# Kernel tuning notes

Measured on AMD Instinct MI355X. Metric: run time of the kernel, lower is better.

The kernel has to match this reference:

```python
import math
import jax, jax.numpy as jnp
import numpy as np

B, S, D, H, M, R = 4, 2048, 512, 8, 4, 32
HD = D // H
EPS = 1e-8


def setup_inputs() -> dict:
    key = jax.random.key(0)
    ks = jax.random.split(key, 12)
    sc = 1.0 / math.sqrt(D)
    return {
        "x": jax.random.normal(ks[0], (B, S, D), jnp.float32),
        "Wq": jax.random.normal(ks[1], (D, D), jnp.float32) * sc,
        "bq": jnp.zeros((D,), jnp.float32),
        "Wk": jax.random.normal(ks[2], (D, D), jnp.float32) * sc,
        "bk": jnp.zeros((D,), jnp.float32),
        "Wv": jax.random.normal(ks[3], (D, D), jnp.float32) * sc,
        "bv": jnp.zeros((D,), jnp.float32),
        "mask1": jax.random.normal(ks[4], (M, R, S), jnp.float32) * (1.0 / math.sqrt(R)),
        "mask2": jax.random.normal(ks[5], (M, R, S), jnp.float32) * (1.0 / math.sqrt(R)),
        "Wo": jax.random.normal(ks[6], (D, D), jnp.float32) * sc,
        "bo": jnp.zeros((D,), jnp.float32),
        "roll_back": jax.random.randint(ks[7], (1, S, S), 0, S, jnp.int32),
    }


def reference(x, Wq, bq, Wk, bk, Wv, bv, mask1, mask2, Wo, bo, roll_back):
    # q, k, v: [B, H, S, HD]  (torch Linear: x @ W.T + b)
    def proj(W, b):
        return (x @ W.T + b).reshape(B, S, H, HD).transpose(0, 2, 1, 3)
    q, k, v = proj(Wq, bq), proj(Wk, bk), proj(Wv, bv)

    # learnable_mask[m,s,t] = sum_r mask1[m,r,s] * mask2[m,r,t]  -> [M, S, S]
    lm = jnp.einsum("mrs,mrt->mst", mask1, mask2)
    # gather along last dim with roll indices expanded to [M, S, S]
    idx = jnp.broadcast_to(roll_back, lm.shape)
    lm_rolled = jnp.take_along_axis(lm, idx, axis=-1)  # [M, S, S]

    # att: [B, H, S, S]
    att = jnp.einsum("bhsd,bhtd->bhst", q, k) / math.sqrt(HD)
    # group heads: [B, H/M, M, S, S] * [1, 1, M, S, S]
    att = att.reshape(B, H // M, M, S, S) * lm_rolled[None, None]
    att = att.reshape(B, H, S, S)

    # Frobenius norm over last two dims, per (batch, head)
    fro = jnp.sqrt(jnp.sum(att * att, axis=(-2, -1), keepdims=True))
    att = att / (fro + EPS)

    out = jnp.einsum("bhst,bhtd->bshd", att, v).reshape(B, S, D)
    return out @ Wo.T + bo
```

## Files before the change

kernel.cpp:

```cpp
#include <hip/hip_runtime.h>
#include <hip/hip_bf16.h>

#define NB 4
#define NS 2048
#define ND 512
#define NH 8
#define NM 4
#define NR 32
#define NHD 64

typedef short frag_ab __attribute__((ext_vector_type(8)));
typedef float frag_cd __attribute__((ext_vector_type(4)));

__device__ __forceinline__ float bf2f(short s) {
    union { unsigned u; float f; } c;
    c.u = ((unsigned)(unsigned short)s) << 16;
    return c.f;
}
__device__ __forceinline__ short f2bf(float f) {
    __hip_bfloat16 h = __float2bfloat16(f);
    union { __hip_bfloat16 h; short s; } c;
    c.h = h;
    return c.s;
}

__device__ __forceinline__ void gload16(const void* g, void* l) {
    __builtin_amdgcn_global_load_lds((const __attribute__((address_space(1))) unsigned int*)g,
                                     (__attribute__((address_space(3))) unsigned int*)l,
                                     16, 0, 0);
}

__device__ __forceinline__ void stage_tile(const short* src, size_t srcStride,
                                           char* lbase, int slot) {
    int o = slot * 16;
    int row = o >> 7;
    int cc = ((o >> 4) & 7) ^ (row & 7);
    gload16(src + (size_t)row * srcStride + cc * 8, lbase + o);
}

__device__ __forceinline__ frag_ab lds_frag(const char* lbase, int row, int cc_un) {
    int cc = cc_un ^ (row & 7);
    return *(const frag_ab*)(lbase + row * 128 + cc * 16);
}

__global__ void __launch_bounds__(256) k_cast(const float* __restrict__ in,
                                              short* __restrict__ out, int n8) {
    int i = blockIdx.x * 256 + threadIdx.x;
    if (i >= n8) return;
    const float4* p = (const float4*)in + (size_t)i * 2;
    float4 a = p[0], b = p[1];
    frag_ab o;
    o[0] = f2bf(a.x); o[1] = f2bf(a.y); o[2] = f2bf(a.z); o[3] = f2bf(a.w);
    o[4] = f2bf(b.x); o[5] = f2bf(b.y); o[6] = f2bf(b.z); o[7] = f2bf(b.w);
    ((frag_ab*)out)[i] = o;
}

__global__ void __launch_bounds__(256) k_castw(const float* __restrict__ Wq,
                                               const float* __restrict__ Wk,
                                               const float* __restrict__ Wv,
                                               const float* __restrict__ Wo,
                                               short* __restrict__ out) {
    int i = blockIdx.x * 256 + threadIdx.x;
    int which = i >> 15;
    int j = i & 32767;
    const float* src = which == 0 ? Wq : which == 1 ? Wk : which == 2 ? Wv : Wo;
    const float4* p = (const float4*)src + (size_t)j * 2;
    float4 a = p[0], b = p[1];
    frag_ab o;
    o[0] = f2bf(a.x); o[1] = f2bf(a.y); o[2] = f2bf(a.z); o[3] = f2bf(a.w);
    o[4] = f2bf(b.x); o[5] = f2bf(b.y); o[6] = f2bf(b.z); o[7] = f2bf(b.w);
    ((frag_ab*)out)[i] = o;
}

__global__ void __launch_bounds__(256) k_tcast_mask(const float* __restrict__ mask1,
                                                    const float* __restrict__ mask2,
                                                    short* __restrict__ m1t,
                                                    short* __restrict__ m2t) {
    int my = blockIdx.y;
    const float* in = my < 4 ? mask1 : mask2;
    short* out = my < 4 ? m1t : m2t;
    int m = my & 3;
    int s0 = blockIdx.x * 64, tid = threadIdx.x;
    __shared__ float tile[32][65];
    int c = tid & 63, r4 = tid >> 6;
#pragma unroll
    for (int p = 0; p < 8; ++p) {
        int r = p * 4 + r4;
        tile[r][c] = in[(m * 32 + r) * NS + s0 + c];
    }
    __syncthreads();
    int r = tid & 31, s4 = tid >> 5;
#pragma unroll
    for (int p = 0; p < 8; ++p) {
        int s = p * 8 + s4;
        out[(m * NS + s0 + s) * NR + r] = f2bf(tile[r][s]);
    }
}

__global__ void __launch_bounds__(256) k_lmroll(const short* __restrict__ m1t,
                                                const short* __restrict__ m2t,
                                                const int* __restrict__ roll,
                                                short* __restrict__ lmr) {
    int n = blockIdx.x;
    int xcd = n & 7, j = n >> 3;
    int m = xcd >> 1;
    int st = (j << 1) | (xcd & 1);
    int s0 = st * 16;
    int tid = threadIdx.x, w = tid >> 6, lane = tid & 63;
    int lo = lane & 15, g = lane >> 4;

    __shared__ __align__(16) char rowbuf_[16 * 4160];

    frag_ab af = *(const frag_ab*)(m1t + (size_t)(m * NS + s0 + lo) * NR + g * 8);
    const short* m2b = m2t + (size_t)m * NS * NR;

    for (int tt = 0; tt < 8; ++tt) {
        int T0 = (w * 8 + tt) * 64;
        frag_cd sacc[4];
#pragma unroll
        for (int ni = 0; ni < 4; ++ni) {
            frag_ab bf = *(const frag_ab*)(m2b + (size_t)(T0 + ni * 16 + lo) * NR + g * 8);
            frag_cd z = {0.f, 0.f, 0.f, 0.f};
            sacc[ni] = __builtin_amdgcn_mfma_f32_16x16x32_bf16(af, bf, z, 0, 0, 0);
        }
        char* pw = rowbuf_ + g * (4 * 4160) + (size_t)(T0 + lo) * 2;
#pragma unroll
        for (int ni = 0; ni < 4; ++ni)
#pragma unroll
            for (int r = 0; r < 4; ++r)
                *(short*)(pw + r * 4160 + ni * 32) = f2bf(sacc[ni][r]);
    }
    __syncthreads();
    int row = w * 4 + (lane >> 4);
    int tbase = (lane & 15) * 8;
    const short* rb = (const short*)(rowbuf_ + row * 4160);
    const int* rrow = roll + (size_t)(s0 + row) * NS;
    short* orow = lmr + ((size_t)(m * NS) + s0 + row) * NS;
#pragma unroll
    for (int c = 0; c < 16; ++c) {
        int t = c * 128 + tbase;
        int4 i0 = *(const int4*)(rrow + t);
        int4 i1 = *(const int4*)(rrow + t + 4);
        frag_ab o;
        o[0] = rb[i0.x]; o[1] = rb[i0.y]; o[2] = rb[i0.z]; o[3] = rb[i0.w];
        o[4] = rb[i1.x]; o[5] = rb[i1.y]; o[6] = rb[i1.z]; o[7] = rb[i1.w];
        *(frag_ab*)(orow + t) = o;
    }
}

__global__ void __launch_bounds__(256) k_gemm_qkv(const short* __restrict__ A,
                                                  const short* __restrict__ Wqb,
                                                  const short* __restrict__ Wkb,
                                                  const short* __restrict__ Wvb,
                                                  const float* __restrict__ bq,
                                                  const float* __restrict__ bk,
                                                  const float* __restrict__ bv,
                                                  short* __restrict__ Qb,
                                                  short* __restrict__ Kb,
                                                  short* __restrict__ Vtb) {
    int n = blockIdx.x;
    int rr = n >> 3;
    int Mb = (n & 7) * 8 + (rr & 7);
    int Nb = rr >> 3;
    int which = Nb >> 3;
    int bn0 = (Nb & 7) * 64;
    const short* W = which == 0 ? Wqb : which == 1 ? Wkb : Wvb;
    const float* bias = which == 0 ? bq : which == 1 ? bk : bv;
    short* out = which == 0 ? Qb : which == 1 ? Kb : Vtb;
    int bm0 = Mb * 128;
    int tid = threadIdx.x;
    int wid = tid >> 6, lane = tid & 63;
    int lo = lane & 15, g = lane >> 4;
    int wr = (wid >> 1) * 64, wc = (wid & 1) * 32;

    __shared__ __align__(16) char sm[2][24576];

    frag_cd acc[4][2];
#pragma unroll
    for (int mi = 0; mi < 4; ++mi)
#pragma unroll
        for (int ni = 0; ni < 2; ++ni) acc[mi][ni] = (frag_cd){0.f, 0.f, 0.f, 0.f};

    const short* Abase = A + (size_t)bm0 * ND;
    const short* Wbase = W + (size_t)bn0 * ND;

#pragma unroll
    for (int j = 0; j < 4; ++j) stage_tile(Abase, ND, sm[0], tid + j * 256);
#pragma unroll
    for (int j = 0; j < 2; ++j) stage_tile(Wbase, ND, sm[0] + 16384, tid + j * 256);
    __syncthreads();

    char* cb = sm[0];
    char* nb = sm[1];
    for (int kt = 0; kt < 8; ++kt) {
        if (kt < 7) {
            int k0 = (kt + 1) * 64;
#pragma unroll
            for (int j = 0; j < 4; ++j) stage_tile(Abase + k0, ND, nb, tid + j * 256);
#pragma unroll
            for (int j = 0; j < 2; ++j) stage_tile(Wbase + k0, ND, nb + 16384, tid + j * 256);
        }
#pragma unroll
        for (int kk = 0; kk < 2; ++kk) {
            frag_ab af[4], bf[2];
#pragma unroll
            for (int mi = 0; mi < 4; ++mi) af[mi] = lds_frag(cb, wr + mi * 16 + lo, kk * 4 + g);
#pragma unroll
            for (int ni = 0; ni < 2; ++ni) bf[ni] = lds_frag(cb + 16384, wc + ni * 16 + lo, kk * 4 + g);
#pragma unroll
            for (int mi = 0; mi < 4; ++mi)
#pragma unroll
                for (int ni = 0; ni < 2; ++ni)
                    acc[mi][ni] = __builtin_amdgcn_mfma_f32_16x16x32_bf16(af[mi], bf[ni], acc[mi][ni], 0, 0, 0);
        }
        __syncthreads();
        char* t = cb; cb = nb; nb = t;
    }

#pragma unroll
    for (int mi = 0; mi < 4; ++mi)
#pragma unroll
        for (int ni = 0; ni < 2; ++ni)
#pragma unroll
            for (int ri = 0; ri < 4; ++ri) {
                int row = bm0 + wr + mi * 16 + g * 4 + ri;
                int col = bn0 + wc + ni * 16 + lo;
                float v = acc[mi][ni][ri] + bias[col];
                if (which == 0) v *= 0.125f;
                int b = row >> 11, s = row & 2047, h = col >> 6, d = col & 63;
                if (which < 2) {
                    out[(((size_t)(b * NH + h) * NS + s) << 6) + d] = f2bf(v);
                } else {
                    out[((size_t)(b * NH + h) * NHD + d) * NS + s] = f2bf(v);
                }
            }
}

__global__ void __launch_bounds__(256) k_gemm_out(const short* __restrict__ A,
                                                  const short* __restrict__ W,
                                                  const float* __restrict__ bias,
                                                  float* __restrict__ out) {
    int n = blockIdx.x;
    int rr = n >> 3;
    int Mb = (n & 7) * 8 + (rr & 7);
    int Nb = rr >> 3;
    int bn0 = Nb * 64;
    int bm0 = Mb * 128;
    int tid = threadIdx.x;
    int wid = tid >> 6, lane = tid & 63;
    int lo = lane & 15, g = lane >> 4;
    int wr = (wid >> 1) * 64, wc = (wid & 1) * 32;

    __shared__ __align__(16) char sm[2][24576];

    frag_cd acc[4][2];
#pragma unroll
    for (int mi = 0; mi < 4; ++mi)
#pragma unroll
        for (int ni = 0; ni < 2; ++ni) acc[mi][ni] = (frag_cd){0.f, 0.f, 0.f, 0.f};

    const short* Abase = A + (size_t)bm0 * ND;
    const short* Wbase = W + (size_t)bn0 * ND;

#pragma unroll
    for (int j = 0; j < 4; ++j) stage_tile(Abase, ND, sm[0], tid + j * 256);
#pragma unroll
    for (int j = 0; j < 2; ++j) stage_tile(Wbase, ND, sm[0] + 16384, tid + j * 256);
    __syncthreads();

    char* cb = sm[0];
    char* nb = sm[1];
    for (int kt = 0; kt < 8; ++kt) {
        if (kt < 7) {
            int k0 = (kt + 1) * 64;
#pragma unroll
            for (int j = 0; j < 4; ++j) stage_tile(Abase + k0, ND, nb, tid + j * 256);
#pragma unroll
            for (int j = 0; j < 2; ++j) stage_tile(Wbase + k0, ND, nb + 16384, tid + j * 256);
        }
#pragma unroll
        for (int kk = 0; kk < 2; ++kk) {
            frag_ab af[4], bf[2];
#pragma unroll
            for (int mi = 0; mi < 4; ++mi) af[mi] = lds_frag(cb, wr + mi * 16 + lo, kk * 4 + g);
#pragma unroll
            for (int ni = 0; ni < 2; ++ni) bf[ni] = lds_frag(cb + 16384, wc + ni * 16 + lo, kk * 4 + g);
#pragma unroll
            for (int mi = 0; mi < 4; ++mi)
#pragma unroll
                for (int ni = 0; ni < 2; ++ni)
                    acc[mi][ni] = __builtin_amdgcn_mfma_f32_16x16x32_bf16(af[mi], bf[ni], acc[mi][ni], 0, 0, 0);
        }
        __syncthreads();
        char* t = cb; cb = nb; nb = t;
    }

#pragma unroll
    for (int mi = 0; mi < 4; ++mi)
#pragma unroll
        for (int ni = 0; ni < 2; ++ni)
#pragma unroll
            for (int ri = 0; ri < 4; ++ri) {
                int row = bm0 + wr + mi * 16 + g * 4 + ri;
                int col = bn0 + wc + ni * 16 + lo;
                out[(size_t)row * ND + col] = acc[mi][ni][ri] + bias[col];
            }
}

__global__ void __launch_bounds__(512, 4) k_attn(const short* __restrict__ Qb,
                                                 const short* __restrict__ Kb,
                                                 const short* __restrict__ Vt,
                                                 const short* __restrict__ lmr,
                                                 short* __restrict__ O,
                                                 float* __restrict__ fro) {
    int n = blockIdx.x;
    int xcd = n & 7;
    int idx = n >> 3;
    int b = idx & 3;
    int hh = (idx >> 2) & 1;
    int sbl = idx >> 3;
    int m = xcd >> 1;
    int sb = (xcd & 1) * 8 + sbl;
    int h = hh * 4 + m;
    int bh = b * NH + h;
    int tid = threadIdx.x;
    int w = tid >> 6, lane = tid & 63;
    int lo = lane & 15, g = lane >> 4;
    int srow = sb * 128 + w * 16;

    __shared__ __align__(16) char kv[2][16384];
    __shared__ __align__(16) char plds[8][4352];
    char* pbase = plds[w];

    const short* kbase = Kb + (size_t)bh * NS * NHD;
    const short* vbase = Vt + (size_t)bh * NHD * NS;
    const short* lmbase = lmr + ((size_t)m * NS + srow + lo) * NS;

    const short* qptr = Qb + ((size_t)bh * NS + srow + lo) * NHD + g * 8;
    frag_ab qf[2];
    qf[0] = *(const frag_ab*)(qptr);
    qf[1] = *(const frag_ab*)(qptr + 32);

    frag_cd acco[4];
#pragma unroll
    for (int ni = 0; ni < 4; ++ni) acco[ni] = (frag_cd){0.f, 0.f, 0.f, 0.f};
    float sumsq = 0.f;

    stage_tile(kbase, NHD, kv[0], tid);
    stage_tile(vbase, NS, kv[0] + 8192, tid);
    frag_ab lc0 = *(const frag_ab*)(lmbase + g * 8);
    frag_ab lc1 = *(const frag_ab*)(lmbase + 32 + g * 8);
    __syncthreads();

    float* pw = (float*)(pbase + g * 1088 + lo * 4);
    const char* prb = pbase + lo * 272 + g * 32;

    char* cb = kv[0];
    char* nb = kv[1];
    for (int tb = 0; tb < 32; ++tb) {
        int t0 = tb * 64;
        frag_ab ln0 = lc0, ln1 = lc1;
        if (tb < 31) {
            stage_tile(kbase + (size_t)(t0 + 64) * NHD, NHD, nb, tid);
            stage_tile(vbase + (t0 + 64), NS, nb + 8192, tid);
            ln0 = *(const frag_ab*)(lmbase + t0 + 64 + g * 8);
            ln1 = *(const frag_ab*)(lmbase + t0 + 96 + g * 8);
        }
        frag_cd sacc[4];
#pragma unroll
        for (int ni = 0; ni < 4; ++ni) sacc[ni] = (frag_cd){0.f, 0.f, 0.f, 0.f};
#pragma unroll
        for (int kk = 0; kk < 2; ++kk)
#pragma unroll
            for (int ni = 0; ni < 4; ++ni)
                sacc[ni] = __builtin_amdgcn_mfma_f32_16x16x32_bf16(
                    qf[kk], lds_frag(cb, ni * 16 + lo, kk * 4 + g), sacc[ni], 0, 0, 0);
#pragma unroll
        for (int ni = 0; ni < 4; ++ni)
#pragma unroll
            for (int r = 0; r < 4; ++r)
                pw[r * 68 + ni * 16] = sacc[ni][r];
        frag_ab pf[2];
#pragma unroll
        for (int kk = 0; kk < 2; ++kk) {
            float4 s0 = *(const float4*)(prb + kk * 128);
            float4 s1 = *(const float4*)(prb + kk * 128 + 16);
            frag_ab lf = kk ? lc1 : lc0;
            float pv[8] = {s0.x, s0.y, s0.z, s0.w, s1.x, s1.y, s1.z, s1.w};
            frag_ab pp;
#pragma unroll
            for (int jj = 0; jj < 8; ++jj) {
                float p = pv[jj] * bf2f(lf[jj]);
                sumsq = fmaf(p, p, sumsq);
                pp[jj] = f2bf(p);
            }
            pf[kk] = pp;
        }
#pragma unroll
        for (int ni = 0; ni < 4; ++ni)
#pragma unroll
            for (int kk = 0; kk < 2; ++kk)
                acco[ni] = __builtin_amdgcn_mfma_f32_16x16x32_bf16(
                    pf[kk], lds_frag(cb + 8192, ni * 16 + lo, kk * 4 + g), acco[ni], 0, 0, 0);
        lc0 = ln0;
        lc1 = ln1;
        __syncthreads();
        char* t = cb; cb = nb; nb = t;
    }
#pragma unroll
    for (int off = 32; off; off >>= 1) sumsq += __shfl_xor(sumsq, off, 64);
    if (lane == 0) atomicAdd(&fro[bh], sumsq);
#pragma unroll
    for (int ni = 0; ni < 4; ++ni)
#pragma unroll
        for (int r = 0; r < 4; ++r) {
            int s = srow + g * 4 + r;
            int d = ni * 16 + lo;
            O[((size_t)(b * NS + s)) * ND + h * NHD + d] = f2bf(acco[ni][r]);
        }
}

__global__ void __launch_bounds__(256) k_scale(short* __restrict__ O,
                                               const float* __restrict__ fro) {
    int i = blockIdx.x * 256 + threadIdx.x;
    int i8 = i * 8;
    int col = i8 & 511;
    int row = i8 >> 9;
    float f = fro[(row >> 11) * NH + (col >> 6)];
    float sc = 1.f / (sqrtf(f) + 1e-8f);
    frag_ab v = ((frag_ab*)O)[i];
    frag_ab o;
#pragma unroll
    for (int j = 0; j < 8; ++j) o[j] = f2bf(bf2f(v[j]) * sc);
    ((frag_ab*)O)[i] = o;
}

extern "C" void kernel_launch(void* const* d_in, const int* in_sizes, int n_in,
                              void* d_out, int out_size, void* d_ws, size_t ws_size,
                              hipStream_t stream) {
    const float* x     = (const float*)d_in[0];
    const float* Wq    = (const float*)d_in[1];
    const float* bq    = (const float*)d_in[2];
    const float* Wk    = (const float*)d_in[3];
    const float* bk    = (const float*)d_in[4];
    const float* Wv    = (const float*)d_in[5];
    const float* bv    = (const float*)d_in[6];
    const float* mask1 = (const float*)d_in[7];
    const float* mask2 = (const float*)d_in[8];
    const float* Wo    = (const float*)d_in[9];
    const float* bo    = (const float*)d_in[10];
    const int*   roll  = (const int*)d_in[11];
    float* out = (float*)d_out;

    char* ws = (char*)d_ws;
    short* xb  = (short*)(ws + 0);
    short* Wqb = (short*)(ws + 8388608);
    short* Wkb = (short*)(ws + 8912896);
    short* Wvb = (short*)(ws + 9437184);
    short* Wob = (short*)(ws + 9961472);
    short* Qb  = (short*)(ws + 10485760);
    short* Kb  = (short*)(ws + 18874368);
    short* Vtb = (short*)(ws + 27262976);
    short* m1t = (short*)(ws + 35651584);
    short* m2t = (short*)(ws + 36175872);
    short* lmr = (short*)(ws + 70254592);
    short* Ob  = (short*)(ws + 103809024);
    float* fro = (float*)(ws + 112197632);

    k_cast<<<2048, 256, 0, stream>>>(x, xb, (NB * NS * ND) / 8);
    k_castw<<<512, 256, 0, stream>>>(Wq, Wk, Wv, Wo, Wqb);
    k_tcast_mask<<<dim3(32, 8), 256, 0, stream>>>(mask1, mask2, m1t, m2t);

    k_lmroll<<<512, 256, 0, stream>>>(m1t, m2t, roll, lmr);

    k_gemm_qkv<<<1536, 256, 0, stream>>>(xb, Wqb, Wkb, Wvb, bq, bk, bv, Qb, Kb, Vtb);

    hipMemsetAsync(fro, 0, 128, stream);
    k_attn<<<512, 512, 0, stream>>>(Qb, Kb, Vtb, lmr, Ob, fro);

    k_scale<<<2048, 256, 0, stream>>>(Ob, fro);
    k_gemm_out<<<512, 256, 0, stream>>>(Ob, Wob, bo, out);
}
```

Before: 232.3 us.

## Keep attention scores in registers by transposing MFMA operands, drop LDS round-trip

Computes the score tile transposed (K fragment as A operand, Q as B) so that each lane's accumulator layout directly matches the B-operand layout of a 16x16x16 bf16 MFMA for the P·V product. This removes the per-wave LDS scratch buffer used to re-layout scores between the two matmuls, along with its stores, loads and shared memory footprint. The mask fragments are loaded as four 4-element vectors and the output is written with vectorized 4-short stores. It trades the 16x16x32 MFMA for twice as many 16x16x16 MFMAs in the PV stage and uses narrower LDS reads for V.

```diff
diff --git a/kernel.cpp b/kernel.cpp
--- a/kernel.cpp
+++ b/kernel.cpp
@@ -10,6 +10,7 @@
 #define NHD 64
 
 typedef short frag_ab __attribute__((ext_vector_type(8)));
+typedef short v4s     __attribute__((ext_vector_type(4)));
 typedef float frag_cd __attribute__((ext_vector_type(4)));
 
 __device__ __forceinline__ float bf2f(short s) {
@@ -41,6 +42,12 @@
 __device__ __forceinline__ frag_ab lds_frag(const char* lbase, int row, int cc_un) {
     int cc = cc_un ^ (row & 7);
     return *(const frag_ab*)(lbase + row * 128 + cc * 16);
+}
+
+__device__ __forceinline__ v4s lds_frag64(const char* lbase, int row, int c0) {
+    int byte = c0 * 2;
+    int cc = (byte >> 4) ^ (row & 7);
+    return *(const v4s*)(lbase + row * 128 + cc * 16 + (byte & 15));
 }
 
 __global__ void __launch_bounds__(256) k_cast(const float* __restrict__ in,
@@ -329,8 +336,6 @@
     int srow = sb * 128 + w * 16;
 
     __shared__ __align__(16) char kv[2][16384];
-    __shared__ __align__(16) char plds[8][4352];
-    char* pbase = plds[w];
 
     const short* kbase = Kb + (size_t)bh * NS * NHD;
     const short* vbase = Vt + (size_t)bh * NHD * NS;
@@ -343,81 +348,75 @@
 
     frag_cd acco[4];
 #pragma unroll
-    for (int ni = 0; ni < 4; ++ni) acco[ni] = (frag_cd){0.f, 0.f, 0.f, 0.f};
+    for (int d = 0; d < 4; ++d) acco[d] = (frag_cd){0.f, 0.f, 0.f, 0.f};
     float sumsq = 0.f;
 
     stage_tile(kbase, NHD, kv[0], tid);
     stage_tile(vbase, NS, kv[0] + 8192, tid);
-    frag_ab lc0 = *(const frag_ab*)(lmbase + g * 8);
-    frag_ab lc1 = *(const frag_ab*)(lmbase + 32 + g * 8);
+    v4s lc0 = *(const v4s*)(lmbase + g * 4);
+    v4s lc1 = *(const v4s*)(lmbase + 16 + g * 4);
+    v4s lc2 = *(const v4s*)(lmbase + 32 + g * 4);
+    v4s lc3 = *(const v4s*)(lmbase + 48 + g * 4);
     __syncthreads();
-
-    float* pw = (float*)(pbase + g * 1088 + lo * 4);
-    const char* prb = pbase + lo * 272 + g * 32;
 
     char* cb = kv[0];
     char* nb = kv[1];
     for (int tb = 0; tb < 32; ++tb) {
         int t0 = tb * 64;
-        frag_ab ln0 = lc0, ln1 = lc1;
+        v4s ln0 = lc0, ln1 = lc1, ln2 = lc2, ln3 = lc3;
         if (tb < 31) {
             stage_tile(kbase + (size_t)(t0 + 64) * NHD, NHD, nb, tid);
             stage_tile(vbase + (t0 + 64), NS, nb + 8192, tid);
-            ln0 = *(const frag_ab*)(lmbase + t0 + 64 + g * 8);
-            ln1 = *(const frag_ab*)(lmbase + t0 + 96 + g * 8);
-        }
-        frag_cd sacc[4];
-#pragma unroll
-        for (int ni = 0; ni < 4; ++ni) sacc[ni] = (frag_cd){0.f, 0.f, 0.f, 0.f};
+            const short* lp = lmbase + t0 + 64;
+            ln0 = *(const v4s*)(lp + g * 4);
+            ln1 = *(const v4s*)(lp + 16 + g * 4);
+            ln2 = *(const v4s*)(lp + 32 + g * 4);
+            ln3 = *(const v4s*)(lp + 48 + g * 4);
+        }
+        frag_cd st[4];
+#pragma unroll
+        for (int blk = 0; blk < 4; ++blk) st[blk] = (frag_cd){0.f, 0.f, 0.f, 0.f};
 #pragma unroll
         for (int kk = 0; kk < 2; ++kk)
 #pragma unroll
-            for (int ni = 0; ni < 4; ++ni)
-                sacc[ni] = __builtin_amdgcn_mfma_f32_16x16x32_bf16(
-                    qf[kk], lds_frag(cb, ni * 16 + lo, kk * 4 + g), sacc[ni], 0, 0, 0);
-#pragma unroll
-        for (int ni = 0; ni < 4; ++ni)
-#pragma unroll
-            for (int r = 0; r < 4; ++r)
-                pw[r * 68 + ni * 16] = sacc[ni][r];
-        frag_ab pf[2];
-#pragma unroll
-        for (int kk = 0; kk < 2; ++kk) {
-            float4 s0 = *(const float4*)(prb + kk * 128);
-            float4 s1 = *(const float4*)(prb + kk * 128 + 16);
-            frag_ab lf = kk ? lc1 : lc0;
-            float pv[8] = {s0.x, s0.y, s0.z, s0.w, s1.x, s1.y, s1.z, s1.w};
-            frag_ab pp;
-#pragma unroll
-            for (int jj = 0; jj < 8; ++jj) {
-                float p = pv[jj] * bf2f(lf[jj]);
-                sumsq = fmaf(p, p, sumsq);
-                pp[jj] = f2bf(p);
+            for (int blk = 0; blk < 4; ++blk)
+                st[blk] = __builtin_amdgcn_mfma_f32_16x16x32_bf16(
+                    lds_frag(cb, blk * 16 + lo, kk * 4 + g), qf[kk], st[blk], 0, 0, 0);
+        v4s pa[4];
+#define PBLK(blk, lcv)                                                        \
+        {                                                                     \
+            float p0 = st[blk][0] * bf2f(lcv[0]);                             \
+            float p1 = st[blk][1] * bf2f(lcv[1]);                             \
+            float p2 = st[blk][2] * bf2f(lcv[2]);                             \
+            float p3 = st[blk][3] * bf2f(lcv[3]);                             \
+            sumsq = fmaf(p0, p0, sumsq); sumsq = fmaf(p1, p1, sumsq);         \
+            sumsq = fmaf(p2, p2, sumsq); sumsq = fmaf(p3, p3, sumsq);         \
+            pa[blk] = (v4s){f2bf(p0), f2bf(p1), f2bf(p2), f2bf(p3)};          \
+        }
+        PBLK(0, lc0) PBLK(1, lc1) PBLK(2, lc2) PBLK(3, lc3)
+#undef PBLK
+#pragma unroll
+        for (int dblk = 0; dblk < 4; ++dblk)
+#pragma unroll
+            for (int kb = 0; kb < 4; ++kb) {
+                v4s vf = lds_frag64(cb + 8192, dblk * 16 + lo, kb * 16 + g * 4);
+                acco[dblk] = __builtin_amdgcn_mfma_f32_16x16x16bf16_1k(
+                    vf, pa[kb], acco[dblk], 0, 0, 0);
             }
-            pf[kk] = pp;
-        }
-#pragma unroll
-        for (int ni = 0; ni < 4; ++ni)
-#pragma unroll
-            for (int kk = 0; kk < 2; ++kk)
-                acco[ni] = __builtin_amdgcn_mfma_f32_16x16x32_bf16(
-                    pf[kk], lds_frag(cb + 8192, ni * 16 + lo, kk * 4 + g), acco[ni], 0, 0, 0);
-        lc0 = ln0;
-        lc1 = ln1;
+        lc0 = ln0; lc1 = ln1; lc2 = ln2; lc3 = ln3;
         __syncthreads();
         char* t = cb; cb = nb; nb = t;
     }
 #pragma unroll
     for (int off = 32; off; off >>= 1) sumsq += __shfl_xor(sumsq, off, 64);
     if (lane == 0) atomicAdd(&fro[bh], sumsq);
-#pragma unroll
-    for (int ni = 0; ni < 4; ++ni)
-#pragma unroll
-        for (int r = 0; r < 4; ++r) {
-            int s = srow + g * 4 + r;
-            int d = ni * 16 + lo;
-            O[((size_t)(b * NS + s)) * ND + h * NHD + d] = f2bf(acco[ni][r]);
-        }
+    short* obase = O + ((size_t)(b * NS) + srow + lo) * ND + h * NHD + g * 4;
+#pragma unroll
+    for (int dblk = 0; dblk < 4; ++dblk) {
+        v4s ov = {f2bf(acco[dblk][0]), f2bf(acco[dblk][1]),
+                  f2bf(acco[dblk][2]), f2bf(acco[dblk][3])};
+        *(v4s*)(obase + dblk * 16) = ov;
+    }
 }
 
 __global__ void __launch_bounds__(256) k_scale(short* __restrict__ O,
```

Measured after the change: 252.4 us. +8.7%, slower.
